# Kernel optimization log

Measured on AMD Instinct MI355X. Metric: run time of the kernel, lower is better.

## Reference

```python
import jax, jax.numpy as jnp
import numpy as np


def setup_inputs() -> dict:
    key = jax.random.key(0)
    kq, kk, kv = jax.random.split(key, 3)
    B, H, L, D = 2, 16, 2048, 64
    Q = jax.random.normal(kq, (B, H, L, D), dtype=jnp.float32)
    K = jax.random.normal(kk, (B, H, L, D), dtype=jnp.float32)
    V = jax.random.normal(kv, (B, H, L, D), dtype=jnp.float32)
    return {"Q": Q, "K": K, "V": V, "topk": 64}


def reference(Q, K, V, topk):
    # dots = Q K^T : [B, H, Lq, Lk]
    dots = jnp.einsum("bhqd,bhkd->bhqk", Q, K)
    B, H, Lq, Lk = dots.shape
    # top-k sparsification along key axis, activation applied only to kept scores
    top_dots, top_inds = jax.lax.top_k(dots, topk)          # [B,H,Lq,topk]
    top_attn = jax.nn.softmax(top_dots, axis=-1)            # activation on top-k scores
    # scatter activated values back into a zero [B,H,Lq,Lk] matrix
    rows = jnp.arange(B * H * Lq)[:, None]
    attn = (
        jnp.zeros((B * H * Lq, Lk), dots.dtype)
        .at[rows, top_inds.reshape(-1, topk)]
        .set(top_attn.reshape(-1, topk))
        .reshape(B, H, Lq, Lk)
    )
    # out = attn V : [B, H, Lq, Dv]
    return jnp.einsum("bhqk,bhkv->bhqv", attn, V)
```

## Files before the change

### kernel.cpp

```cpp
#include <hip/hip_runtime.h>

typedef _Float16 half8_t __attribute__((ext_vector_type(8)));
typedef _Float16 half4_t __attribute__((ext_vector_type(4)));
typedef float    f32x4   __attribute__((ext_vector_type(4)));

#define LSEQ    2048
#define DIM     64
#define ROWS    16
#define TOPK    64
#define CAP     128
#define NROWTOT 65536
#define SCSTR   (LSEQ + 8)

static __device__ __forceinline__ _Float16 u16_as_h(unsigned short u) {
    union { unsigned short u; _Float16 h; } c; c.u = u; return c.h;
}

__global__ void cvt_f16_kernel(const float* __restrict__ Q, const float* __restrict__ K,
                               _Float16* __restrict__ Q16, _Float16* __restrict__ K16, int n4)
{
    int i = blockIdx.x * blockDim.x + threadIdx.x;
    if (i >= n4) return;
    float4 q = reinterpret_cast<const float4*>(Q)[i];
    float4 k = reinterpret_cast<const float4*>(K)[i];
    half4_t hq = { (_Float16)q.x, (_Float16)q.y, (_Float16)q.z, (_Float16)q.w };
    half4_t hk = { (_Float16)k.x, (_Float16)k.y, (_Float16)k.z, (_Float16)k.w };
    reinterpret_cast<half4_t*>(Q16)[i] = hq;
    reinterpret_cast<half4_t*>(K16)[i] = hk;
}

template <bool PRE>
__global__ __launch_bounds__(512) __attribute__((amdgpu_waves_per_eu(4, 4)))
void topk_attn_kernel(
    const float* __restrict__ Qf, const float* __restrict__ Kf, const float* __restrict__ Vf,
    const _Float16* __restrict__ Q16, const _Float16* __restrict__ K16,
    float* __restrict__ Out)
{
    __shared__ _Float16 sc[ROWS][SCSTR];
    __shared__ float    qlds[ROWS][DIM];
    __shared__ int      candIdx[8][CAP];
    __shared__ int      pvK[8][TOPK];
    __shared__ float    pvW[8][TOPK];

    const int tid  = threadIdx.x;
    const int wave = tid >> 6;
    const int lane = tid & 63;

    const long rowbase  = (long)blockIdx.x * ROWS;
    const long headbase = (rowbase >> 11) << 11;

    for (int i = tid; i < ROWS * DIM; i += 512)
        qlds[i >> 6][i & 63] = Qf[rowbase * DIM + i];

    const int g = lane >> 4;
    const int r = lane & 15;

    half8_t a0, a1;
    if constexpr (PRE) {
        a0 = *reinterpret_cast<const half8_t*>(Q16 + (rowbase + r) * DIM + g * 8);
        a1 = *reinterpret_cast<const half8_t*>(Q16 + (rowbase + r) * DIM + 32 + g * 8);
    } else {
        const float* qp = Qf + (rowbase + r) * DIM + g * 8;
        #pragma unroll
        for (int j = 0; j < 8; ++j) { a0[j] = (_Float16)qp[j]; a1[j] = (_Float16)qp[32 + j]; }
    }

    #pragma unroll 4
    for (int t = 0; t < 16; ++t) {
        const int key = t * 128 + wave * 16 + r;
        half8_t b0, b1;
        if constexpr (PRE) {
            const _Float16* kp = K16 + (headbase + key) * DIM + g * 8;
            b0 = *reinterpret_cast<const half8_t*>(kp);
            b1 = *reinterpret_cast<const half8_t*>(kp + 32);
        } else {
            const float* kp = Kf + (headbase + key) * DIM + g * 8;
            #pragma unroll
            for (int j = 0; j < 8; ++j) { b0[j] = (_Float16)kp[j]; b1[j] = (_Float16)kp[32 + j]; }
        }
        f32x4 acc = {0.f, 0.f, 0.f, 0.f};
        acc = __builtin_amdgcn_mfma_f32_16x16x32_f16(a0, b0, acc, 0, 0, 0);
        acc = __builtin_amdgcn_mfma_f32_16x16x32_f16(a1, b1, acc, 0, 0, 0);
        #pragma unroll
        for (int j = 0; j < 4; ++j)
            sc[g * 4 + j][key] = (_Float16)acc[j];
    }
    __syncthreads();

    const unsigned long long mlt = (1ull << lane) - 1ull;
    const int perm = lane & 3;

    for (int rr = 0; rr < 2; ++rr) {
        const int row = wave * 2 + rr;

        const half8_t* sp = reinterpret_cast<const half8_t*>(&sc[row][lane * 32]);
        half8_t h[4];
        h[0] = sp[0 ^ perm];
        h[1] = sp[1 ^ perm];
        h[2] = sp[2 ^ perm];
        h[3] = sp[3 ^ perm];

        unsigned cut16 = 0u;
        for (int b = 15; b >= 0; --b) {
            const unsigned trial = cut16 | (1u << b);
            const unsigned short tb = (trial & 0x8000u)
                                        ? (unsigned short)(trial ^ 0x8000u)
                                        : (unsigned short)(~trial);
            const _Float16 T = u16_as_h(tb);
            int cnt = 0;
            #pragma unroll
            for (int i = 0; i < 4; ++i)
                #pragma unroll
                for (int e = 0; e < 8; ++e)
                    cnt += __popcll(__ballot(h[i][e] >= T));
            if (cnt >= TOPK) cut16 = trial;
        }
        const unsigned short cb = (cut16 & 0x8000u)
                                    ? (unsigned short)(cut16 ^ 0x8000u)
                                    : (unsigned short)(~cut16);
        const float H64 = (float)u16_as_h(cb);
        const _Float16 hTf = (_Float16)(H64 - 0.35f);

        int total = 0;
        #pragma unroll
        for (int i = 0; i < 4; ++i)
            #pragma unroll
            for (int e = 0; e < 8; ++e) {
                const bool c = (h[i][e] >= hTf);
                const unsigned long long b = __ballot(c);
                const int pos = total + __popcll(b & mlt);
                if (c && pos < CAP)
                    candIdx[wave][pos] = lane * 32 + ((i ^ perm) << 3) + e;
                total += __popcll(b);
            }
        int nAll = (total > CAP) ? CAP : total;
        asm volatile("s_waitcnt lgkmcnt(0)" ::: "memory");

        float ex[2]; unsigned us[2]; int ci[2];
        #pragma unroll
        for (int p = 0; p < 2; ++p) {
            const int c = lane + 64 * p;
            const bool valid = (c < nAll);
            const int key = valid ? candIdx[wave][c] : 0;
            ci[p] = key;
            float dot = 0.f;
            const float4* kp4 = reinterpret_cast<const float4*>(Kf + (headbase + key) * DIM);
            #pragma unroll
            for (int chk = 0; chk < 16; ++chk) {
                const float4 kk = kp4[chk];
                dot = fmaf(kk.x, qlds[row][chk * 4 + 0], dot);
                dot = fmaf(kk.y, qlds[row][chk * 4 + 1], dot);
                dot = fmaf(kk.z, qlds[row][chk * 4 + 2], dot);
                dot = fmaf(kk.w, qlds[row][chk * 4 + 3], dot);
            }
            ex[p] = dot;
            unsigned u = __float_as_uint(dot);
            u ^= (unsigned)((int)u >> 31) | 0x80000000u;
            us[p] = valid ? u : 0u;
        }

        unsigned cut = 0u;
        #pragma unroll
        for (int b = 31; b >= 0; --b) {
            const unsigned trial = cut | (1u << b);
            const int cnt = __popcll(__ballot(us[0] >= trial)) +
                            __popcll(__ballot(us[1] >= trial));
            if (cnt >= TOPK) cut = trial;
        }

        const unsigned long long beq0 = __ballot(us[0] == cut);
        const unsigned long long beq1 = __ballot(us[1] == cut);
        const int cntGt = __popcll(__ballot(us[0] > cut)) + __popcll(__ballot(us[1] > cut));
        const int need  = TOPK - cntGt;
        const int rank0 = __popcll(beq0 & mlt);
        const int rank1 = __popcll(beq0) + __popcll(beq1 & mlt);
        const bool sel0 = (us[0] > cut) || ((us[0] == cut) && (rank0 < need));
        const bool sel1 = (us[1] > cut) || ((us[1] == cut) && (rank1 < need));

        float mxe = fmaxf(sel0 ? ex[0] : -1e30f, sel1 ? ex[1] : -1e30f);
        #pragma unroll
        for (int o = 32; o > 0; o >>= 1) mxe = fmaxf(mxe, __shfl_xor(mxe, o));
        const float w0 = sel0 ? expf(ex[0] - mxe) : 0.f;
        const float w1 = sel1 ? expf(ex[1] - mxe) : 0.f;
        float zs = w0 + w1;
        #pragma unroll
        for (int o = 32; o > 0; o >>= 1) zs += __shfl_xor(zs, o);
        const float inv = 1.f / zs;

        pvK[wave][lane] = 0;
        pvW[wave][lane] = 0.f;
        const unsigned long long bs0 = __ballot(sel0);
        const unsigned long long bs1 = __ballot(sel1);
        const int pos0 = __popcll(bs0 & mlt);
        const int pos1 = __popcll(bs0) + __popcll(bs1 & mlt);
        if (sel0) { pvK[wave][pos0] = ci[0]; pvW[wave][pos0] = w0 * inv; }
        if (sel1) { pvK[wave][pos1] = ci[1]; pvW[wave][pos1] = w1 * inv; }
        asm volatile("s_waitcnt lgkmcnt(0)" ::: "memory");

        float acc = 0.f;
        #pragma unroll 16
        for (int i = 0; i < TOPK; ++i) {
            const int   ki = pvK[wave][i];
            const float wi = pvW[wave][i];
            acc = fmaf(wi, Vf[(headbase + ki) * DIM + lane], acc);
        }
        Out[(rowbase + row) * DIM + lane] = acc;
    }
}

extern "C" void kernel_launch(void* const* d_in, const int* in_sizes, int n_in,
                              void* d_out, int out_size, void* d_ws, size_t ws_size,
                              hipStream_t stream)
{
    const float* Q = (const float*)d_in[0];
    const float* K = (const float*)d_in[1];
    const float* V = (const float*)d_in[2];
    float* Out = (float*)d_out;

    const int nElem = 2 * 16 * 2048 * 64;
    const size_t needWs = (size_t)2 * (size_t)nElem * sizeof(_Float16);

    if (ws_size >= needWs) {
        _Float16* Q16 = (_Float16*)d_ws;
        _Float16* K16 = Q16 + nElem;
        cvt_f16_kernel<<<(nElem / 4) / 256, 256, 0, stream>>>(Q, K, Q16, K16, nElem / 4);
        topk_attn_kernel<true><<<NROWTOT / ROWS, 512, 0, stream>>>(Q, K, V, Q16, K16, Out);
    } else {
        topk_attn_kernel<false><<<NROWTOT / ROWS, 512, 0, stream>>>(Q, K, V, nullptr, nullptr, Out);
    }
}
```

Measured before the change: 802.2 us.

## Halve rows per block, one row per wave, swizzle blocks across XCDs

Reduces each block to 8 query rows so every wave processes a single row, doubling the grid and raising the waves-per-EU target. Block indices are remapped so consecutive blocks of the same head land on the same XCD for better L2 reuse of K. The fp16 prefilter margin is tightened to shrink the candidate set. In exchange, half of each MFMA tile is wasted and K tiles are loaded twice as often per row, and the narrower margin risks missing true top-k keys.

```diff
diff --git a/kernel.cpp b/kernel.cpp
--- a/kernel.cpp
+++ b/kernel.cpp
@@ -6,10 +6,11 @@
 
 #define LSEQ    2048
 #define DIM     64
-#define ROWS    16
+#define ROWS    8
 #define TOPK    64
 #define CAP     128
 #define NROWTOT 65536
+#define NBLK    (NROWTOT / ROWS)
 #define SCSTR   (LSEQ + 8)
 
 static __device__ __forceinline__ _Float16 u16_as_h(unsigned short u) {
@@ -30,7 +31,7 @@
 }
 
 template <bool PRE>
-__global__ __launch_bounds__(512) __attribute__((amdgpu_waves_per_eu(4, 4)))
+__global__ __launch_bounds__(512) __attribute__((amdgpu_waves_per_eu(6, 6)))
 void topk_attn_kernel(
     const float* __restrict__ Qf, const float* __restrict__ Kf, const float* __restrict__ Vf,
     const _Float16* __restrict__ Q16, const _Float16* __restrict__ K16,
@@ -46,21 +47,25 @@
     const int wave = tid >> 6;
     const int lane = tid & 63;
 
-    const long rowbase  = (long)blockIdx.x * ROWS;
+    const int p = blockIdx.x;
+    const int logical = (p & 7) * (NBLK / 8) + (p >> 3);
+
+    const long rowbase  = (long)logical * ROWS;
     const long headbase = (rowbase >> 11) << 11;
 
-    for (int i = tid; i < ROWS * DIM; i += 512)
-        qlds[i >> 6][i & 63] = Qf[rowbase * DIM + i];
+    if (tid < ROWS * DIM)
+        qlds[tid >> 6][tid & 63] = Qf[rowbase * DIM + tid];
 
     const int g = lane >> 4;
     const int r = lane & 15;
 
+    const int qrow = r & 7;
     half8_t a0, a1;
     if constexpr (PRE) {
-        a0 = *reinterpret_cast<const half8_t*>(Q16 + (rowbase + r) * DIM + g * 8);
-        a1 = *reinterpret_cast<const half8_t*>(Q16 + (rowbase + r) * DIM + 32 + g * 8);
+        a0 = *reinterpret_cast<const half8_t*>(Q16 + (rowbase + qrow) * DIM + g * 8);
+        a1 = *reinterpret_cast<const half8_t*>(Q16 + (rowbase + qrow) * DIM + 32 + g * 8);
     } else {
-        const float* qp = Qf + (rowbase + r) * DIM + g * 8;
+        const float* qp = Qf + (rowbase + qrow) * DIM + g * 8;
         #pragma unroll
         for (int j = 0; j < 8; ++j) { a0[j] = (_Float16)qp[j]; a1[j] = (_Float16)qp[32 + j]; }
     }
@@ -81,131 +86,130 @@
         f32x4 acc = {0.f, 0.f, 0.f, 0.f};
         acc = __builtin_amdgcn_mfma_f32_16x16x32_f16(a0, b0, acc, 0, 0, 0);
         acc = __builtin_amdgcn_mfma_f32_16x16x32_f16(a1, b1, acc, 0, 0, 0);
-        #pragma unroll
-        for (int j = 0; j < 4; ++j)
-            sc[g * 4 + j][key] = (_Float16)acc[j];
+        if (g < 2) {
+            #pragma unroll
+            for (int j = 0; j < 4; ++j)
+                sc[g * 4 + j][key] = (_Float16)acc[j];
+        }
     }
     __syncthreads();
 
     const unsigned long long mlt = (1ull << lane) - 1ull;
     const int perm = lane & 3;
-
-    for (int rr = 0; rr < 2; ++rr) {
-        const int row = wave * 2 + rr;
-
-        const half8_t* sp = reinterpret_cast<const half8_t*>(&sc[row][lane * 32]);
-        half8_t h[4];
-        h[0] = sp[0 ^ perm];
-        h[1] = sp[1 ^ perm];
-        h[2] = sp[2 ^ perm];
-        h[3] = sp[3 ^ perm];
-
-        unsigned cut16 = 0u;
-        for (int b = 15; b >= 0; --b) {
-            const unsigned trial = cut16 | (1u << b);
-            const unsigned short tb = (trial & 0x8000u)
-                                        ? (unsigned short)(trial ^ 0x8000u)
-                                        : (unsigned short)(~trial);
-            const _Float16 T = u16_as_h(tb);
-            int cnt = 0;
-            #pragma unroll
-            for (int i = 0; i < 4; ++i)
-                #pragma unroll
-                for (int e = 0; e < 8; ++e)
-                    cnt += __popcll(__ballot(h[i][e] >= T));
-            if (cnt >= TOPK) cut16 = trial;
-        }
-        const unsigned short cb = (cut16 & 0x8000u)
-                                    ? (unsigned short)(cut16 ^ 0x8000u)
-                                    : (unsigned short)(~cut16);
-        const float H64 = (float)u16_as_h(cb);
-        const _Float16 hTf = (_Float16)(H64 - 0.35f);
-
-        int total = 0;
+    const int row  = wave;
+
+    const half8_t* sp = reinterpret_cast<const half8_t*>(&sc[row][lane * 32]);
+    half8_t h[4];
+    h[0] = sp[0 ^ perm];
+    h[1] = sp[1 ^ perm];
+    h[2] = sp[2 ^ perm];
+    h[3] = sp[3 ^ perm];
+
+    unsigned cut16 = 0u;
+    for (int b = 15; b >= 0; --b) {
+        const unsigned trial = cut16 | (1u << b);
+        const unsigned short tb = (trial & 0x8000u)
+                                    ? (unsigned short)(trial ^ 0x8000u)
+                                    : (unsigned short)(~trial);
+        const _Float16 T = u16_as_h(tb);
+        int cnt = 0;
         #pragma unroll
         for (int i = 0; i < 4; ++i)
             #pragma unroll
-            for (int e = 0; e < 8; ++e) {
-                const bool c = (h[i][e] >= hTf);
-                const unsigned long long b = __ballot(c);
-                const int pos = total + __popcll(b & mlt);
-                if (c && pos < CAP)
-                    candIdx[wave][pos] = lane * 32 + ((i ^ perm) << 3) + e;
-                total += __popcll(b);
-            }
-        int nAll = (total > CAP) ? CAP : total;
-        asm volatile("s_waitcnt lgkmcnt(0)" ::: "memory");
-
-        float ex[2]; unsigned us[2]; int ci[2];
-        #pragma unroll
-        for (int p = 0; p < 2; ++p) {
-            const int c = lane + 64 * p;
-            const bool valid = (c < nAll);
-            const int key = valid ? candIdx[wave][c] : 0;
-            ci[p] = key;
-            float dot = 0.f;
-            const float4* kp4 = reinterpret_cast<const float4*>(Kf + (headbase + key) * DIM);
-            #pragma unroll
-            for (int chk = 0; chk < 16; ++chk) {
-                const float4 kk = kp4[chk];
-                dot = fmaf(kk.x, qlds[row][chk * 4 + 0], dot);
-                dot = fmaf(kk.y, qlds[row][chk * 4 + 1], dot);
-                dot = fmaf(kk.z, qlds[row][chk * 4 + 2], dot);
-                dot = fmaf(kk.w, qlds[row][chk * 4 + 3], dot);
-            }
-            ex[p] = dot;
-            unsigned u = __float_as_uint(dot);
-            u ^= (unsigned)((int)u >> 31) | 0x80000000u;
-            us[p] = valid ? u : 0u;
-        }
-
-        unsigned cut = 0u;
-        #pragma unroll
-        for (int b = 31; b >= 0; --b) {
-            const unsigned trial = cut | (1u << b);
-            const int cnt = __popcll(__ballot(us[0] >= trial)) +
-                            __popcll(__ballot(us[1] >= trial));
-            if (cnt >= TOPK) cut = trial;
-        }
-
-        const unsigned long long beq0 = __ballot(us[0] == cut);
-        const unsigned long long beq1 = __ballot(us[1] == cut);
-        const int cntGt = __popcll(__ballot(us[0] > cut)) + __popcll(__ballot(us[1] > cut));
-        const int need  = TOPK - cntGt;
-        const int rank0 = __popcll(beq0 & mlt);
-        const int rank1 = __popcll(beq0) + __popcll(beq1 & mlt);
-        const bool sel0 = (us[0] > cut) || ((us[0] == cut) && (rank0 < need));
-        const bool sel1 = (us[1] > cut) || ((us[1] == cut) && (rank1 < need));
-
-        float mxe = fmaxf(sel0 ? ex[0] : -1e30f, sel1 ? ex[1] : -1e30f);
-        #pragma unroll
-        for (int o = 32; o > 0; o >>= 1) mxe = fmaxf(mxe, __shfl_xor(mxe, o));
-        const float w0 = sel0 ? expf(ex[0] - mxe) : 0.f;
-        const float w1 = sel1 ? expf(ex[1] - mxe) : 0.f;
-        float zs = w0 + w1;
-        #pragma unroll
-        for (int o = 32; o > 0; o >>= 1) zs += __shfl_xor(zs, o);
-        const float inv = 1.f / zs;
-
-        pvK[wave][lane] = 0;
-        pvW[wave][lane] = 0.f;
-        const unsigned long long bs0 = __ballot(sel0);
-        const unsigned long long bs1 = __ballot(sel1);
-        const int pos0 = __popcll(bs0 & mlt);
-        const int pos1 = __popcll(bs0) + __popcll(bs1 & mlt);
-        if (sel0) { pvK[wave][pos0] = ci[0]; pvW[wave][pos0] = w0 * inv; }
-        if (sel1) { pvK[wave][pos1] = ci[1]; pvW[wave][pos1] = w1 * inv; }
-        asm volatile("s_waitcnt lgkmcnt(0)" ::: "memory");
-
-        float acc = 0.f;
-        #pragma unroll 16
-        for (int i = 0; i < TOPK; ++i) {
-            const int   ki = pvK[wave][i];
-            const float wi = pvW[wave][i];
-            acc = fmaf(wi, Vf[(headbase + ki) * DIM + lane], acc);
-        }
-        Out[(rowbase + row) * DIM + lane] = acc;
-    }
+            for (int e = 0; e < 8; ++e)
+                cnt += __popcll(__ballot(h[i][e] >= T));
+        if (cnt >= TOPK) cut16 = trial;
+    }
+    const unsigned short cb = (cut16 & 0x8000u)
+                                ? (unsigned short)(cut16 ^ 0x8000u)
+                                : (unsigned short)(~cut16);
+    const float H64 = (float)u16_as_h(cb);
+    const _Float16 hTf = (_Float16)(H64 - 0.25f);
+
+    int total = 0;
+    #pragma unroll
+    for (int i = 0; i < 4; ++i)
+        #pragma unroll
+        for (int e = 0; e < 8; ++e) {
+            const bool c = (h[i][e] >= hTf);
+            const unsigned long long b = __ballot(c);
+            const int pos = total + __popcll(b & mlt);
+            if (c && pos < CAP)
+                candIdx[wave][pos] = lane * 32 + ((i ^ perm) << 3) + e;
+            total += __popcll(b);
+        }
+    int nAll = (total > CAP) ? CAP : total;
+    asm volatile("s_waitcnt lgkmcnt(0)" ::: "memory");
+
+    float ex[2]; unsigned us[2]; int ci[2];
+    #pragma unroll
+    for (int pp = 0; pp < 2; ++pp) {
+        const int c = lane + 64 * pp;
+        const bool valid = (c < nAll);
+        const int key = valid ? candIdx[wave][c] : 0;
+        ci[pp] = key;
+        float dot = 0.f;
+        const float4* kp4 = reinterpret_cast<const float4*>(Kf + (headbase + key) * DIM);
+        #pragma unroll
+        for (int chk = 0; chk < 16; ++chk) {
+            const float4 kk = kp4[chk];
+            dot = fmaf(kk.x, qlds[row][chk * 4 + 0], dot);
+            dot = fmaf(kk.y, qlds[row][chk * 4 + 1], dot);
+            dot = fmaf(kk.z, qlds[row][chk * 4 + 2], dot);
+            dot = fmaf(kk.w, qlds[row][chk * 4 + 3], dot);
+        }
+        ex[pp] = dot;
+        unsigned u = __float_as_uint(dot);
+        u ^= (unsigned)((int)u >> 31) | 0x80000000u;
+        us[pp] = valid ? u : 0u;
+    }
+
+    unsigned cut = 0u;
+    #pragma unroll
+    for (int b = 31; b >= 0; --b) {
+        const unsigned trial = cut | (1u << b);
+        const int cnt = __popcll(__ballot(us[0] >= trial)) +
+                        __popcll(__ballot(us[1] >= trial));
+        if (cnt >= TOPK) cut = trial;
+    }
+
+    const unsigned long long beq0 = __ballot(us[0] == cut);
+    const unsigned long long beq1 = __ballot(us[1] == cut);
+    const int cntGt = __popcll(__ballot(us[0] > cut)) + __popcll(__ballot(us[1] > cut));
+    const int need  = TOPK - cntGt;
+    const int rank0 = __popcll(beq0 & mlt);
+    const int rank1 = __popcll(beq0) + __popcll(beq1 & mlt);
+    const bool sel0 = (us[0] > cut) || ((us[0] == cut) && (rank0 < need));
+    const bool sel1 = (us[1] > cut) || ((us[1] == cut) && (rank1 < need));
+
+    float mxe = fmaxf(sel0 ? ex[0] : -1e30f, sel1 ? ex[1] : -1e30f);
+    #pragma unroll
+    for (int o = 32; o > 0; o >>= 1) mxe = fmaxf(mxe, __shfl_xor(mxe, o));
+    const float w0 = sel0 ? expf(ex[0] - mxe) : 0.f;
+    const float w1 = sel1 ? expf(ex[1] - mxe) : 0.f;
+    float zs = w0 + w1;
+    #pragma unroll
+    for (int o = 32; o > 0; o >>= 1) zs += __shfl_xor(zs, o);
+    const float inv = 1.f / zs;
+
+    pvK[wave][lane] = 0;
+    pvW[wave][lane] = 0.f;
+    const unsigned long long bs0 = __ballot(sel0);
+    const unsigned long long bs1 = __ballot(sel1);
+    const int pos0 = __popcll(bs0 & mlt);
+    const int pos1 = __popcll(bs0) + __popcll(bs1 & mlt);
+    if (sel0) { pvK[wave][pos0] = ci[0]; pvW[wave][pos0] = w0 * inv; }
+    if (sel1) { pvK[wave][pos1] = ci[1]; pvW[wave][pos1] = w1 * inv; }
+    asm volatile("s_waitcnt lgkmcnt(0)" ::: "memory");
+
+    float acc = 0.f;
+    #pragma unroll 16
+    for (int i = 0; i < TOPK; ++i) {
+        const int   ki = pvK[wave][i];
+        const float wi = pvW[wave][i];
+        acc = fmaf(wi, Vf[(headbase + ki) * DIM + lane], acc);
+    }
+    Out[(rowbase + row) * DIM + lane] = acc;
 }
 
 extern "C" void kernel_launch(void* const* d_in, const int* in_sizes, int n_in,
@@ -224,8 +228,8 @@
         _Float16* Q16 = (_Float16*)d_ws;
         _Float16* K16 = Q16 + nElem;
         cvt_f16_kernel<<<(nElem / 4) / 256, 256, 0, stream>>>(Q, K, Q16, K16, nElem / 4);
-        topk_attn_kernel<true><<<NROWTOT / ROWS, 512, 0, stream>>>(Q, K, V, Q16, K16, Out);
+        topk_attn_kernel<true><<<NBLK, 512, 0, stream>>>(Q, K, V, Q16, K16, Out);
     } else {
-        topk_attn_kernel<false><<<NROWTOT / ROWS, 512, 0, stream>>>(Q, K, V, nullptr, nullptr, Out);
-    }
-}
+        topk_attn_kernel<false><<<NBLK, 512, 0, stream>>>(Q, K, V, nullptr, nullptr, Out);
+    }
+}
```

Result: slower. 848.8 us (+5.8%).
